# Kernel optimization log

Hardware: AMD Instinct MI355X
Metric: run time of the kernel (lower is better)

## Reference

```python
import jax, jax.numpy as jnp
import numpy as np

N = 100000      # nodes
E = 1600000     # edges (before self-loops)
IN_DIM = 128
HEADS = 4
C = 32          # hid_dim // heads = 128 // 4
SLOPE = 0.2     # PyG GATConv default negative_slope


def setup_inputs() -> dict:
    key = jax.random.key(0)
    k1, k2, k3, k4, k5 = jax.random.split(key, 5)
    x = jax.random.normal(k1, (N, IN_DIM), dtype=jnp.float32)
    edge_index = jax.random.randint(k2, (2, E), 0, N, dtype=jnp.int32)
    # learned parameters of GATConv
    W = jax.random.normal(k3, (IN_DIM, HEADS * C), dtype=jnp.float32) / np.sqrt(IN_DIM)
    att_src = jax.random.normal(k4, (HEADS, C), dtype=jnp.float32) * 0.1
    att_dst = jax.random.normal(k5, (HEADS, C), dtype=jnp.float32) * 0.1
    bias = jnp.zeros((HEADS * C,), dtype=jnp.float32)
    return {"x": x, "edge_index": edge_index, "W": W,
            "att_src": att_src, "att_dst": att_dst, "bias": bias}


def reference(x, edge_index, W, att_src, att_dst, bias):
    # PyG GATConv default add_self_loops=True
    loops = jnp.arange(N, dtype=edge_index.dtype)
    ei = jnp.concatenate([edge_index, jnp.stack([loops, loops])], axis=1)
    src, dst = ei[0], ei[1]                       # messages flow src -> dst

    h = (x @ W).reshape(N, HEADS, C)              # [N,H,C]
    a_src = jnp.einsum('nhc,hc->nh', h, att_src)  # [N,H]
    a_dst = jnp.einsum('nhc,hc->nh', h, att_dst)  # [N,H]

    e = a_src[src] + a_dst[dst]                   # [E+N,H] per-edge logits
    e = jax.nn.leaky_relu(e, SLOPE)

    # segment softmax over edges sharing a destination node
    m = jax.ops.segment_max(e, dst, num_segments=N)        # [N,H]
    e = jnp.exp(e - m[dst])
    s = jax.ops.segment_sum(e, dst, num_segments=N)        # [N,H]
    alpha = e / (s[dst] + 1e-16)                            # [E+N,H]

    msg = h[src] * alpha[:, :, None]                        # [E+N,H,C]
    out = jax.ops.segment_sum(msg, dst, num_segments=N)     # [N,H,C]
    return out.reshape(N, HEADS * C) + bias                 # concat heads + bias
```

## Files before the change

### kernel.cpp

```cpp
#include <hip/hip_runtime.h>
#include <cstddef>

#define HEADS 4
#define HC 128
#define SLOPE 0.2f
#define NPBUCK 256
#define NSBMAX 512
#define SBCAP 5120
#define CHUNK 4096
#define GTILE 128

using half8 = __attribute__((ext_vector_type(8))) _Float16;
using f32x4 = __attribute__((ext_vector_type(4))) float;

__device__ __forceinline__ float edge_w(float v) {
    v = v > 0.f ? v : SLOPE * v;
    return __expf(v);
}
__device__ __forceinline__ float2 up2(unsigned w) {
    union { unsigned u; _Float16 f[2]; } c; c.u = w;
    return make_float2((float)c.f[0], (float)c.f[1]);
}

__global__ void wt_kernel(const float* __restrict__ W,
                          const float* __restrict__ att_src,
                          const float* __restrict__ att_dst,
                          _Float16* __restrict__ WTh,
                          _Float16* __restrict__ WAttT,
                          int* __restrict__ cursor) {
    int k = threadIdx.x;
    int nn = blockIdx.x;
    WTh[nn * HC + k] = (_Float16)W[k * HC + nn];
    if (nn < 4) {
        int b = nn * 128 + k;
        cursor[b] = b * SBCAP;
    }
    if (nn == 0) {
#pragma unroll
        for (int head = 0; head < 4; ++head) {
            float s = 0.f, d = 0.f;
#pragma unroll
            for (int c = 0; c < 32; ++c) {
                float w = W[k * HC + head * 32 + c];
                s += w * att_src[head * 32 + c];
                d += w * att_dst[head * 32 + c];
            }
            WAttT[head * HC + k]       = (_Float16)s;
            WAttT[(4 + head) * HC + k] = (_Float16)d;
        }
#pragma unroll
        for (int r = 8; r < 16; ++r) WAttT[r * HC + k] = (_Float16)0.f;
    }
}

__global__ __launch_bounds__(256)
void gemm_att_kernel(const float* __restrict__ x, const _Float16* __restrict__ WTh,
                     const _Float16* __restrict__ WAttT,
                     _Float16* __restrict__ h2,
                     float* __restrict__ a_s, float* __restrict__ a_d, int n) {
    __shared__ _Float16 lA[GTILE * HC];
    __shared__ _Float16 lB[HC * HC];
    __shared__ _Float16 lAtt[16 * HC];
    int tid = threadIdx.x;

    int r0 = blockIdx.x * GTILE;
#pragma unroll
    for (int it = 0; it < 16; ++it) {
        int idx = it * 256 + tid;
        int r   = idx >> 5;
        int c8  = idx & 31;
        int rowg = r0 + r; if (rowg >= n) rowg = n - 1;
        float4 f = *(const float4*)(x + (size_t)rowg * HC + c8 * 4);
        union { _Float16 h[4]; uint2 u; } pk;
        pk.h[0] = (_Float16)f.x; pk.h[1] = (_Float16)f.y;
        pk.h[2] = (_Float16)f.z; pk.h[3] = (_Float16)f.w;
        int byte = r * 256 + (((c8 >> 1) ^ (r & 15)) << 4) + ((c8 & 1) << 3);
        *(uint2*)((char*)lA + byte) = pk.u;
    }
#pragma unroll
    for (int it = 0; it < 8; ++it) {
        int idx = it * 256 + tid;
        int r = idx >> 4, c = idx & 15;
        uint4 v = *(const uint4*)(WTh + (size_t)r * HC + c * 8);
        *(uint4*)((char*)lB + r * 256 + ((c ^ (r & 15)) << 4)) = v;
    }
    {
        int r = tid >> 4, c = tid & 15;
        uint4 v = *(const uint4*)(WAttT + (size_t)r * HC + c * 8);
        *(uint4*)((char*)lAtt + r * 256 + ((c ^ r) << 4)) = v;
    }
    __syncthreads();

    int wv   = tid >> 6;
    int lane = tid & 63;
    int t    = lane & 15;
    int q    = lane >> 4;

    f32x4 acc[2][8];
    f32x4 accA[2];
#pragma unroll
    for (int rt = 0; rt < 2; ++rt) {
        accA[rt] = (f32x4){0.f, 0.f, 0.f, 0.f};
#pragma unroll
        for (int ct = 0; ct < 8; ++ct) acc[rt][ct] = (f32x4){0.f, 0.f, 0.f, 0.f};
    }

    int ar0 = wv * 32 + t;
    int ar1 = ar0 + 16;
#pragma unroll
    for (int kc = 0; kc < 4; ++kc) {
        int c = kc * 4 + q;
        half8 a0 = *(const half8*)((char*)lA + ar0 * 256 + ((c ^ t) << 4));
        half8 a1 = *(const half8*)((char*)lA + ar1 * 256 + ((c ^ t) << 4));
#pragma unroll
        for (int ct = 0; ct < 8; ++ct) {
            int rb = ct * 16 + t;
            half8 b = *(const half8*)((char*)lB + rb * 256 + ((c ^ t) << 4));
            acc[0][ct] = __builtin_amdgcn_mfma_f32_16x16x32_f16(a0, b, acc[0][ct], 0, 0, 0);
            acc[1][ct] = __builtin_amdgcn_mfma_f32_16x16x32_f16(a1, b, acc[1][ct], 0, 0, 0);
        }
        half8 bA = *(const half8*)((char*)lAtt + t * 256 + ((c ^ t) << 4));
        accA[0] = __builtin_amdgcn_mfma_f32_16x16x32_f16(a0, bA, accA[0], 0, 0, 0);
        accA[1] = __builtin_amdgcn_mfma_f32_16x16x32_f16(a1, bA, accA[1], 0, 0, 0);
    }

#pragma unroll
    for (int rt = 0; rt < 2; ++rt) {
        int Rbase = r0 + wv * 32 + rt * 16;
#pragma unroll
        for (int reg = 0; reg < 4; ++reg) {
            int row = Rbase + q * 4 + reg;
            if (row < n) {
#pragma unroll
                for (int ct = 0; ct < 8; ++ct)
                    h2[(size_t)row * HC + ct * 16 + t] = (_Float16)acc[rt][ct][reg];
            }
        }
#pragma unroll
        for (int reg = 0; reg < 4; ++reg) {
            int row = Rbase + q * 4 + reg;
            if (row < n && t < 8) {
                if (t < 4) a_s[(size_t)row * 4 + t]       = accA[rt][reg];
                else       a_d[(size_t)row * 4 + (t - 4)] = accA[rt][reg];
            }
        }
    }
}

__global__ __launch_bounds__(256)
void scatter_kernel(const int* __restrict__ ei, int E, int n,
                    int* __restrict__ cursor, int* __restrict__ binned) {
    __shared__ int cnt[NSBMAX];
    __shared__ int lstart[NSBMAX];
    __shared__ int pos[256];
    __shared__ int gbase[NSBMAX];
    __shared__ int valA[CHUNK];
    __shared__ unsigned short bkA[CHUNK];
    int tid = threadIdx.x;
    int Etot = E + n;
    int e0 = blockIdx.x * CHUNK;
    int eend = e0 + CHUNK; if (eend > Etot) eend = Etot;
    int tot = eend - e0;

    for (int i = tid; i < NSBMAX; i += 256) cnt[i] = 0;
    __syncthreads();

    int esv[CHUNK / 256]; int edv[CHUNK / 256];
#pragma unroll
    for (int it = 0; it < CHUNK / 256; ++it) {
        int e = e0 + it * 256 + tid;
        int src = 0, dst = 0;
        if (e < Etot) {
            if (e < E) { src = ei[e]; dst = ei[E + e]; }
            else       { src = e - E; dst = src; }
            atomicAdd(&cnt[dst >> 8], 1);
        }
        esv[it] = src; edv[it] = dst;
    }
    __syncthreads();

    for (int i = tid; i < NSBMAX; i += 256) {
        int c = cnt[i];
        gbase[i] = (c > 0) ? atomicAdd(&cursor[i], c) : 0;
    }

    int c0 = cnt[2 * tid], c1 = cnt[2 * tid + 1];
    int p = c0 + c1;
    pos[tid] = p;
    __syncthreads();
#pragma unroll
    for (int off = 1; off < 256; off <<= 1) {
        int v = (tid >= off) ? pos[tid - off] : 0;
        __syncthreads();
        pos[tid] += v;
        __syncthreads();
    }
    int excl = pos[tid] - p;
    lstart[2 * tid]     = excl;
    lstart[2 * tid + 1] = excl + c0;
    __syncthreads();

    for (int i = tid; i < NSBMAX; i += 256) cnt[i] = lstart[i];
    __syncthreads();
#pragma unroll
    for (int it = 0; it < CHUNK / 256; ++it) {
        int e = e0 + it * 256 + tid;
        if (e < Etot) {
            int bk = edv[it] >> 8;
            int lp = atomicAdd(&cnt[bk], 1);
            valA[lp] = esv[it] | ((edv[it] & 255) << 17);
            bkA[lp] = (unsigned short)bk;
        }
    }
    __syncthreads();

    for (int j = tid; j < tot; j += 256) {
        int b = bkA[j];
        binned[gbase[b] + (j - lstart[b])] = valA[j];
    }
}

__global__ __launch_bounds__(256)
void place_kernel(const int* __restrict__ bucketend, const int* __restrict__ binned,
                  int* __restrict__ sorted, int* __restrict__ rowstart,
                  int* __restrict__ deg, int n) {
    __shared__ int win[SBCAP];
    __shared__ int cnt[256];
    __shared__ int pos[256];
    int b = blockIdx.x;
    int dst0 = b << 8;
    int rows = n - dst0; if (rows > 256) rows = 256;
    int tid = threadIdx.x;
    int wstart = b * SBCAP;
    int tot = bucketend[b] - wstart;

    cnt[tid] = 0;
    __syncthreads();
    for (int j = tid; j < tot; j += 256) {
        int v = binned[wstart + j];
        win[j] = v;
        atomicAdd(&cnt[v >> 17], 1);
    }
    __syncthreads();

    int d = cnt[tid];
    pos[tid] = d;
    __syncthreads();
#pragma unroll
    for (int off = 1; off < 256; off <<= 1) {
        int v = (tid >= off) ? pos[tid - off] : 0;
        __syncthreads();
        pos[tid] += v;
        __syncthreads();
    }
    int excl = pos[tid] - d;
    if (tid < rows) {
        rowstart[dst0 + tid] = wstart + excl;
        deg[dst0 + tid] = d;
    }
    cnt[tid] = excl;
    __syncthreads();
    for (int j = tid; j < tot; j += 256) {
        int v = win[j];
        int p = atomicAdd(&cnt[v >> 17], 1);
        sorted[wstart + p] = v & 0x1FFFF;
    }
}

__global__ __launch_bounds__(256)
void agg_kernel(const int* __restrict__ rowstart, const int* __restrict__ deg,
                const int* __restrict__ sorted,
                const float* __restrict__ a_s, const float* __restrict__ a_d,
                const _Float16* __restrict__ h2, const float* __restrict__ bias,
                float* __restrict__ out, int n) {
    int dst = blockIdx.x * 4 + (threadIdx.x >> 6);
    if (dst >= n) return;
    int lane = threadIdx.x & 63;
    int li   = lane & 15;
    int sub  = lane >> 4;
    int head = li >> 2;
    int start = rowstart[dst];
    int cntv  = deg[dst];

    float ad = a_d[(size_t)dst * 4 + head];
    const uint4* h4 = (const uint4*)h2;
    float acc[8] = {0.f,0.f,0.f,0.f,0.f,0.f,0.f,0.f};
    float wsum = 0.f;

    for (int j = 0; j < cntv; j += 16) {
        int   sv[4]; float wv[4]; uint4 hv[4];
#pragma unroll
        for (int k = 0; k < 4; ++k) {
            int idx = j + k * 4 + sub;
            bool valid = idx < cntv;
            sv[k] = sorted[start + (valid ? idx : cntv - 1)];
            wv[k] = valid ? 1.f : 0.f;
        }
#pragma unroll
        for (int k = 0; k < 4; ++k)
            hv[k] = h4[(size_t)sv[k] * 16 + li];
#pragma unroll
        for (int k = 0; k < 4; ++k) {
            float w = wv[k] * edge_w(a_s[(size_t)sv[k] * 4 + head] + ad);
            float2 f0 = up2(hv[k].x), f1 = up2(hv[k].y),
                   f2 = up2(hv[k].z), f3 = up2(hv[k].w);
            acc[0] = fmaf(w, f0.x, acc[0]); acc[1] = fmaf(w, f0.y, acc[1]);
            acc[2] = fmaf(w, f1.x, acc[2]); acc[3] = fmaf(w, f1.y, acc[3]);
            acc[4] = fmaf(w, f2.x, acc[4]); acc[5] = fmaf(w, f2.y, acc[5]);
            acc[6] = fmaf(w, f3.x, acc[6]); acc[7] = fmaf(w, f3.y, acc[7]);
            wsum += w;
        }
    }

#pragma unroll
    for (int k = 0; k < 8; ++k) {
        acc[k] += __shfl_xor(acc[k], 16);
        acc[k] += __shfl_xor(acc[k], 32);
    }
    wsum += __shfl_xor(wsum, 16);
    wsum += __shfl_xor(wsum, 32);

    if (sub == 0) {
        float inv = 1.f / wsum;
        float4 b0 = ((const float4*)bias)[li * 2];
        float4 b1 = ((const float4*)bias)[li * 2 + 1];
        float4 o0 = make_float4(acc[0]*inv + b0.x, acc[1]*inv + b0.y,
                                acc[2]*inv + b0.z, acc[3]*inv + b0.w);
        float4 o1 = make_float4(acc[4]*inv + b1.x, acc[5]*inv + b1.y,
                                acc[6]*inv + b1.z, acc[7]*inv + b1.w);
        float4* op = (float4*)(out + (size_t)dst * HC);
        op[li * 2]     = o0;
        op[li * 2 + 1] = o1;
    }
}

extern "C" void kernel_launch(void* const* d_in, const int* in_sizes, int n_in,
                              void* d_out, int out_size, void* d_ws, size_t ws_size,
                              hipStream_t stream) {
    const float* x       = (const float*)d_in[0];
    const int*   ei      = (const int*)d_in[1];
    const float* W       = (const float*)d_in[2];
    const float* att_src = (const float*)d_in[3];
    const float* att_dst = (const float*)d_in[4];
    const float* bias    = (const float*)d_in[5];

    int n = in_sizes[0] / HC;
    int E = in_sizes[1] / 2;
    int Etot = E + n;
    int nbuck   = (n + NPBUCK - 1) / NPBUCK;
    int nchunks = (Etot + CHUNK - 1) / CHUNK;
    int gb      = (n + GTILE - 1) / GTILE;

    _Float16* h2     = (_Float16*)d_ws;
    _Float16* WTh    = h2 + (size_t)n * HC;
    _Float16* WAttT  = WTh + HC * HC;
    float* a_s       = (float*)(WAttT + 16 * HC);
    float* a_d       = a_s + (size_t)n * HEADS;
    int*   cursor    = (int*)(a_d + (size_t)n * HEADS);
    int*   rowstart  = cursor + NSBMAX;
    int*   deg       = rowstart + n;
    int*   binned    = deg + n;
    int*   sorted    = binned + (size_t)nbuck * SBCAP;
    float* out       = (float*)d_out;

    wt_kernel<<<HC, HC, 0, stream>>>(W, att_src, att_dst, WTh, WAttT, cursor);
    gemm_att_kernel<<<gb, 256, 0, stream>>>(x, WTh, WAttT, h2, a_s, a_d, n);
    scatter_kernel<<<nchunks, 256, 0, stream>>>(ei, E, n, cursor, binned);
    place_kernel<<<nbuck, 256, 0, stream>>>(cursor, binned, sorted,
                                            rowstart, deg, n);
    agg_kernel<<<(n + 3) / 4, 256, 0, stream>>>(rowstart, deg, sorted,
                                                a_s, a_d, h2, bias, out, n);
}
```

Measured before the change: 230.6 us.

## Replace two-level bucket sort with degree count, scan and direct atomic scatter

Replaces the LDS-staged bucket binning and per-bucket placement with a per-node degree count using global atomics, a per-bucket exclusive scan into fixed SBCAP windows, and a direct scatter where each edge takes a slot through an atomic on its destination's cursor. This removes the intermediate binned array and the shared-memory staging passes, but it reads the edge list twice and issues about 1.7M global atomics spread across 100K addresses. The order of edges within a row becomes nondeterministic.

```diff
diff --git a/kernel.cpp b/kernel.cpp
--- a/kernel.cpp
+++ b/kernel.cpp
@@ -7,7 +7,6 @@
 #define NPBUCK 256
 #define NSBMAX 512
 #define SBCAP 5120
-#define CHUNK 4096
 #define GTILE 128
 
 using half8 = __attribute__((ext_vector_type(8))) _Float16;
@@ -27,14 +26,11 @@
                           const float* __restrict__ att_dst,
                           _Float16* __restrict__ WTh,
                           _Float16* __restrict__ WAttT,
-                          int* __restrict__ cursor) {
+                          int* __restrict__ deg, int n) {
     int k = threadIdx.x;
     int nn = blockIdx.x;
     WTh[nn * HC + k] = (_Float16)W[k * HC + nn];
-    if (nn < 4) {
-        int b = nn * 128 + k;
-        cursor[b] = b * SBCAP;
-    }
+    for (int i = nn * HC + k; i < n; i += HC * HC) deg[i] = 0;
     if (nn == 0) {
 #pragma unroll
         for (int head = 0; head < 4; ++head) {
@@ -50,6 +46,43 @@
         }
 #pragma unroll
         for (int r = 8; r < 16; ++r) WAttT[r * HC + k] = (_Float16)0.f;
+    }
+}
+
+__global__ __launch_bounds__(256)
+void degcnt_kernel(const int* __restrict__ ei, int E, int n,
+                   int* __restrict__ deg) {
+    int idx = blockIdx.x * 256 + threadIdx.x;
+    int stride = gridDim.x * 256;
+    int Etot = E + n;
+    for (int e = idx; e < Etot; e += stride) {
+        int dst = (e < E) ? ei[E + e] : (e - E);
+        atomicAdd(&deg[dst], 1);
+    }
+}
+
+__global__ __launch_bounds__(256)
+void rowscan_kernel(const int* __restrict__ deg, int* __restrict__ rowstart,
+                    int* __restrict__ cursor, int n) {
+    __shared__ int pos[256];
+    int b = blockIdx.x;
+    int tid = threadIdx.x;
+    int dst = (b << 8) + tid;
+    int d = (dst < n) ? deg[dst] : 0;
+    pos[tid] = d;
+    __syncthreads();
+#pragma unroll
+    for (int off = 1; off < 256; off <<= 1) {
+        int v = (tid >= off) ? pos[tid - off] : 0;
+        __syncthreads();
+        pos[tid] += v;
+        __syncthreads();
+    }
+    int excl = pos[tid] - d;
+    if (dst < n) {
+        int p = b * SBCAP + excl;
+        rowstart[dst] = p;
+        cursor[dst]   = p;
     }
 }
 
@@ -148,122 +181,17 @@
 }
 
 __global__ __launch_bounds__(256)
-void scatter_kernel(const int* __restrict__ ei, int E, int n,
-                    int* __restrict__ cursor, int* __restrict__ binned) {
-    __shared__ int cnt[NSBMAX];
-    __shared__ int lstart[NSBMAX];
-    __shared__ int pos[256];
-    __shared__ int gbase[NSBMAX];
-    __shared__ int valA[CHUNK];
-    __shared__ unsigned short bkA[CHUNK];
-    int tid = threadIdx.x;
+void scatter_direct_kernel(const int* __restrict__ ei, int E, int n,
+                           int* __restrict__ cursor, int* __restrict__ sorted) {
+    int idx = blockIdx.x * 256 + threadIdx.x;
+    int stride = gridDim.x * 256;
     int Etot = E + n;
-    int e0 = blockIdx.x * CHUNK;
-    int eend = e0 + CHUNK; if (eend > Etot) eend = Etot;
-    int tot = eend - e0;
-
-    for (int i = tid; i < NSBMAX; i += 256) cnt[i] = 0;
-    __syncthreads();
-
-    int esv[CHUNK / 256]; int edv[CHUNK / 256];
-#pragma unroll
-    for (int it = 0; it < CHUNK / 256; ++it) {
-        int e = e0 + it * 256 + tid;
-        int src = 0, dst = 0;
-        if (e < Etot) {
-            if (e < E) { src = ei[e]; dst = ei[E + e]; }
-            else       { src = e - E; dst = src; }
-            atomicAdd(&cnt[dst >> 8], 1);
-        }
-        esv[it] = src; edv[it] = dst;
-    }
-    __syncthreads();
-
-    for (int i = tid; i < NSBMAX; i += 256) {
-        int c = cnt[i];
-        gbase[i] = (c > 0) ? atomicAdd(&cursor[i], c) : 0;
-    }
-
-    int c0 = cnt[2 * tid], c1 = cnt[2 * tid + 1];
-    int p = c0 + c1;
-    pos[tid] = p;
-    __syncthreads();
-#pragma unroll
-    for (int off = 1; off < 256; off <<= 1) {
-        int v = (tid >= off) ? pos[tid - off] : 0;
-        __syncthreads();
-        pos[tid] += v;
-        __syncthreads();
-    }
-    int excl = pos[tid] - p;
-    lstart[2 * tid]     = excl;
-    lstart[2 * tid + 1] = excl + c0;
-    __syncthreads();
-
-    for (int i = tid; i < NSBMAX; i += 256) cnt[i] = lstart[i];
-    __syncthreads();
-#pragma unroll
-    for (int it = 0; it < CHUNK / 256; ++it) {
-        int e = e0 + it * 256 + tid;
-        if (e < Etot) {
-            int bk = edv[it] >> 8;
-            int lp = atomicAdd(&cnt[bk], 1);
-            valA[lp] = esv[it] | ((edv[it] & 255) << 17);
-            bkA[lp] = (unsigned short)bk;
-        }
-    }
-    __syncthreads();
-
-    for (int j = tid; j < tot; j += 256) {
-        int b = bkA[j];
-        binned[gbase[b] + (j - lstart[b])] = valA[j];
-    }
-}
-
-__global__ __launch_bounds__(256)
-void place_kernel(const int* __restrict__ bucketend, const int* __restrict__ binned,
-                  int* __restrict__ sorted, int* __restrict__ rowstart,
-                  int* __restrict__ deg, int n) {
-    __shared__ int win[SBCAP];
-    __shared__ int cnt[256];
-    __shared__ int pos[256];
-    int b = blockIdx.x;
-    int dst0 = b << 8;
-    int rows = n - dst0; if (rows > 256) rows = 256;
-    int tid = threadIdx.x;
-    int wstart = b * SBCAP;
-    int tot = bucketend[b] - wstart;
-
-    cnt[tid] = 0;
-    __syncthreads();
-    for (int j = tid; j < tot; j += 256) {
-        int v = binned[wstart + j];
-        win[j] = v;
-        atomicAdd(&cnt[v >> 17], 1);
-    }
-    __syncthreads();
-
-    int d = cnt[tid];
-    pos[tid] = d;
-    __syncthreads();
-#pragma unroll
-    for (int off = 1; off < 256; off <<= 1) {
-        int v = (tid >= off) ? pos[tid - off] : 0;
-        __syncthreads();
-        pos[tid] += v;
-        __syncthreads();
-    }
-    int excl = pos[tid] - d;
-    if (tid < rows) {
-        rowstart[dst0 + tid] = wstart + excl;
-        deg[dst0 + tid] = d;
-    }
-    cnt[tid] = excl;
-    __syncthreads();
-    for (int j = tid; j < tot; j += 256) {
-        int v = win[j];
-        int p = atomicAdd(&cnt[v >> 17], 1);
-        sorted[wstart + p] = v & 0x1FFFF;
+    for (int e = idx; e < Etot; e += stride) {
+        int src, dst;
+        if (e < E) { src = ei[e]; dst = ei[E + e]; }
+        else       { src = e - E; dst = src; }
+        int p = atomicAdd(&cursor[dst], 1);
+        sorted[p] = src;
     }
 }
 
@@ -346,9 +274,7 @@
 
     int n = in_sizes[0] / HC;
     int E = in_sizes[1] / 2;
-    int Etot = E + n;
     int nbuck   = (n + NPBUCK - 1) / NPBUCK;
-    int nchunks = (Etot + CHUNK - 1) / CHUNK;
     int gb      = (n + GTILE - 1) / GTILE;
 
     _Float16* h2     = (_Float16*)d_ws;
@@ -356,18 +282,17 @@
     _Float16* WAttT  = WTh + HC * HC;
     float* a_s       = (float*)(WAttT + 16 * HC);
     float* a_d       = a_s + (size_t)n * HEADS;
-    int*   cursor    = (int*)(a_d + (size_t)n * HEADS);
-    int*   rowstart  = cursor + NSBMAX;
-    int*   deg       = rowstart + n;
-    int*   binned    = deg + n;
-    int*   sorted    = binned + (size_t)nbuck * SBCAP;
+    int*   deg       = (int*)(a_d + (size_t)n * HEADS);
+    int*   rowstart  = deg + n;
+    int*   cursor    = rowstart + n;
+    int*   sorted    = cursor + n;
     float* out       = (float*)d_out;
 
-    wt_kernel<<<HC, HC, 0, stream>>>(W, att_src, att_dst, WTh, WAttT, cursor);
+    wt_kernel<<<HC, HC, 0, stream>>>(W, att_src, att_dst, WTh, WAttT, deg, n);
+    degcnt_kernel<<<1024, 256, 0, stream>>>(ei, E, n, deg);
     gemm_att_kernel<<<gb, 256, 0, stream>>>(x, WTh, WAttT, h2, a_s, a_d, n);
-    scatter_kernel<<<nchunks, 256, 0, stream>>>(ei, E, n, cursor, binned);
-    place_kernel<<<nbuck, 256, 0, stream>>>(cursor, binned, sorted,
-                                            rowstart, deg, n);
+    rowscan_kernel<<<nbuck, 256, 0, stream>>>(deg, rowstart, cursor, n);
+    scatter_direct_kernel<<<1024, 256, 0, stream>>>(ei, E, n, cursor, sorted);
     agg_kernel<<<(n + 3) / 4, 256, 0, stream>>>(rowstart, deg, sorted,
                                                 a_s, a_d, h2, bias, out, n);
 }
```

Result: slower. 378.3 us (+64.1%).

## Merge GEMM and edge-scatter kernels into one launch with block-range dispatch

Applied to the files above, without the earlier changes.

Combines the feature GEMM/attention kernel and the edge binning scatter kernel into a single launch, where blocks past the GEMM grid run the scatter work and reuse the GEMM's shared-memory buffers. This removes one kernel launch and lets the two independent phases overlap on the GPU. The cost is that scatter blocks are now held to the GEMM's large shared-memory footprint, which lowers their occupancy compared with the standalone scatter kernel.

```diff
diff --git a/kernel.cpp b/kernel.cpp
--- a/kernel.cpp
+++ b/kernel.cpp
@@ -54,14 +54,90 @@
 }
 
 __global__ __launch_bounds__(256)
-void gemm_att_kernel(const float* __restrict__ x, const _Float16* __restrict__ WTh,
-                     const _Float16* __restrict__ WAttT,
-                     _Float16* __restrict__ h2,
-                     float* __restrict__ a_s, float* __restrict__ a_d, int n) {
+void gemm_att_scatter_kernel(const float* __restrict__ x,
+                             const _Float16* __restrict__ WTh,
+                             const _Float16* __restrict__ WAttT,
+                             _Float16* __restrict__ h2,
+                             float* __restrict__ a_s, float* __restrict__ a_d,
+                             const int* __restrict__ ei,
+                             int* __restrict__ cursor, int* __restrict__ binned,
+                             int gb, int E, int n) {
     __shared__ _Float16 lA[GTILE * HC];
     __shared__ _Float16 lB[HC * HC];
     __shared__ _Float16 lAtt[16 * HC];
     int tid = threadIdx.x;
+
+    if (blockIdx.x >= gb) {
+        int*            valA   = (int*)lA;
+        unsigned short* bkA    = (unsigned short*)((char*)lA + 16384);
+        int*            cnt    = (int*)((char*)lA + 24576);
+        int*            lstart = (int*)((char*)lA + 26624);
+        int*            gbase  = (int*)((char*)lA + 28672);
+        int*            pos    = (int*)lB;
+        int cb = blockIdx.x - gb;
+        int Etot = E + n;
+        int e0 = cb * CHUNK;
+        int eend = e0 + CHUNK; if (eend > Etot) eend = Etot;
+        int tot = eend - e0;
+
+        for (int i = tid; i < NSBMAX; i += 256) cnt[i] = 0;
+        __syncthreads();
+
+        int esv[CHUNK / 256]; int edv[CHUNK / 256];
+#pragma unroll
+        for (int it = 0; it < CHUNK / 256; ++it) {
+            int e = e0 + it * 256 + tid;
+            int src = 0, dst = 0;
+            if (e < Etot) {
+                if (e < E) { src = ei[e]; dst = ei[E + e]; }
+                else       { src = e - E; dst = src; }
+                atomicAdd(&cnt[dst >> 8], 1);
+            }
+            esv[it] = src; edv[it] = dst;
+        }
+        __syncthreads();
+
+        for (int i = tid; i < NSBMAX; i += 256) {
+            int c = cnt[i];
+            gbase[i] = (c > 0) ? atomicAdd(&cursor[i], c) : 0;
+        }
+
+        int c0 = cnt[2 * tid], c1 = cnt[2 * tid + 1];
+        int p = c0 + c1;
+        pos[tid] = p;
+        __syncthreads();
+#pragma unroll
+        for (int off = 1; off < 256; off <<= 1) {
+            int v = (tid >= off) ? pos[tid - off] : 0;
+            __syncthreads();
+            pos[tid] += v;
+            __syncthreads();
+        }
+        int excl = pos[tid] - p;
+        lstart[2 * tid]     = excl;
+        lstart[2 * tid + 1] = excl + c0;
+        __syncthreads();
+
+        for (int i = tid; i < NSBMAX; i += 256) cnt[i] = lstart[i];
+        __syncthreads();
+#pragma unroll
+        for (int it = 0; it < CHUNK / 256; ++it) {
+            int e = e0 + it * 256 + tid;
+            if (e < Etot) {
+                int bk = edv[it] >> 8;
+                int lp = atomicAdd(&cnt[bk], 1);
+                valA[lp] = esv[it] | ((edv[it] & 255) << 17);
+                bkA[lp] = (unsigned short)bk;
+            }
+        }
+        __syncthreads();
+
+        for (int j = tid; j < tot; j += 256) {
+            int b = bkA[j];
+            binned[gbase[b] + (j - lstart[b])] = valA[j];
+        }
+        return;
+    }
 
     int r0 = blockIdx.x * GTILE;
 #pragma unroll
@@ -144,79 +220,6 @@
                 else       a_d[(size_t)row * 4 + (t - 4)] = accA[rt][reg];
             }
         }
-    }
-}
-
-__global__ __launch_bounds__(256)
-void scatter_kernel(const int* __restrict__ ei, int E, int n,
-                    int* __restrict__ cursor, int* __restrict__ binned) {
-    __shared__ int cnt[NSBMAX];
-    __shared__ int lstart[NSBMAX];
-    __shared__ int pos[256];
-    __shared__ int gbase[NSBMAX];
-    __shared__ int valA[CHUNK];
-    __shared__ unsigned short bkA[CHUNK];
-    int tid = threadIdx.x;
-    int Etot = E + n;
-    int e0 = blockIdx.x * CHUNK;
-    int eend = e0 + CHUNK; if (eend > Etot) eend = Etot;
-    int tot = eend - e0;
-
-    for (int i = tid; i < NSBMAX; i += 256) cnt[i] = 0;
-    __syncthreads();
-
-    int esv[CHUNK / 256]; int edv[CHUNK / 256];
-#pragma unroll
-    for (int it = 0; it < CHUNK / 256; ++it) {
-        int e = e0 + it * 256 + tid;
-        int src = 0, dst = 0;
-        if (e < Etot) {
-            if (e < E) { src = ei[e]; dst = ei[E + e]; }
-            else       { src = e - E; dst = src; }
-            atomicAdd(&cnt[dst >> 8], 1);
-        }
-        esv[it] = src; edv[it] = dst;
-    }
-    __syncthreads();
-
-    for (int i = tid; i < NSBMAX; i += 256) {
-        int c = cnt[i];
-        gbase[i] = (c > 0) ? atomicAdd(&cursor[i], c) : 0;
-    }
-
-    int c0 = cnt[2 * tid], c1 = cnt[2 * tid + 1];
-    int p = c0 + c1;
-    pos[tid] = p;
-    __syncthreads();
-#pragma unroll
-    for (int off = 1; off < 256; off <<= 1) {
-        int v = (tid >= off) ? pos[tid - off] : 0;
-        __syncthreads();
-        pos[tid] += v;
-        __syncthreads();
-    }
-    int excl = pos[tid] - p;
-    lstart[2 * tid]     = excl;
-    lstart[2 * tid + 1] = excl + c0;
-    __syncthreads();
-
-    for (int i = tid; i < NSBMAX; i += 256) cnt[i] = lstart[i];
-    __syncthreads();
-#pragma unroll
-    for (int it = 0; it < CHUNK / 256; ++it) {
-        int e = e0 + it * 256 + tid;
-        if (e < Etot) {
-            int bk = edv[it] >> 8;
-            int lp = atomicAdd(&cnt[bk], 1);
-            valA[lp] = esv[it] | ((edv[it] & 255) << 17);
-            bkA[lp] = (unsigned short)bk;
-        }
-    }
-    __syncthreads();
-
-    for (int j = tid; j < tot; j += 256) {
-        int b = bkA[j];
-        binned[gbase[b] + (j - lstart[b])] = valA[j];
     }
 }
 
@@ -364,8 +367,8 @@
     float* out       = (float*)d_out;
 
     wt_kernel<<<HC, HC, 0, stream>>>(W, att_src, att_dst, WTh, WAttT, cursor);
-    gemm_att_kernel<<<gb, 256, 0, stream>>>(x, WTh, WAttT, h2, a_s, a_d, n);
-    scatter_kernel<<<nchunks, 256, 0, stream>>>(ei, E, n, cursor, binned);
+    gemm_att_scatter_kernel<<<gb + nchunks, 256, 0, stream>>>(
+        x, WTh, WAttT, h2, a_s, a_d, ei, cursor, binned, gb, E, n);
     place_kernel<<<nbuck, 256, 0, stream>>>(cursor, binned, sorted,
                                             rowstart, deg, n);
     agg_kernel<<<(n + 3) / 4, 256, 0, stream>>>(rowstart, deg, sorted,
```

After: 224.6 us. 1.03x faster.
